# Kernel optimization log

Measured on AMD Instinct MI355X. Metric: run time of the kernel, lower is better.

Reference implementation:

```python
import jax, jax.numpy as jnp
import numpy as np

N = 50000
E = 800000
EL = 100000
IN_CH = 33
HID = 64
OUT = 128
NTYPES = 311
EMB = 16
COMB = IN_CH - 1 + EMB  # 48


def setup_inputs() -> dict:
    key = jax.random.key(0)
    ks = jax.random.split(key, 24)
    # x: col 0 = node type (integer-valued float), rest = float features
    types = jax.random.randint(ks[0], (N, 1), 0, NTYPES).astype(jnp.float32)
    feats = jax.random.normal(ks[1], (N, IN_CH - 1), dtype=jnp.float32)
    x = jnp.concatenate([types, feats], axis=1)
    edge_index = jax.random.randint(ks[2], (2, E), 0, N, dtype=jnp.int32)
    edge_label_index = jax.random.randint(ks[3], (2, EL), 0, N, dtype=jnp.int32)
    s = 0.05
    inp = {
        'x': x, 'edge_index': edge_index, 'edge_label_index': edge_label_index,
        'emb': jax.random.normal(ks[4], (NTYPES, EMB)) * s,
        'W1': jax.random.normal(ks[5], (COMB, 4 * HID)) * s,
        'a_src1': jax.random.normal(ks[6], (4, HID)) * s,
        'a_dst1': jax.random.normal(ks[7], (4, HID)) * s,
        'b1': jnp.zeros((4 * HID,)),
        'W2': jax.random.normal(ks[8], (4 * HID, 2 * 2 * HID)) * s,
        'a_src2': jax.random.normal(ks[9], (2, 2 * HID)) * s,
        'a_dst2': jax.random.normal(ks[10], (2, 2 * HID)) * s,
        'b2': jnp.zeros((2 * 2 * HID,)),
        'W3': jax.random.normal(ks[11], (4 * HID, OUT)) * s,
        'a_src3': jax.random.normal(ks[12], (1, OUT)) * s,
        'a_dst3': jax.random.normal(ks[13], (1, OUT)) * s,
        'b3': jnp.zeros((OUT,)),
        'Wl1': jax.random.normal(ks[14], (2 * OUT, HID)) * s,
        'bl1': jnp.zeros((HID,)),
        'Wl2': jax.random.normal(ks[15], (HID, 1)) * s,
        'bl2': jnp.zeros((1,)),
        'trans_bias': jax.random.normal(ks[16], (NTYPES, NTYPES)) * s,
    }
    return inp


def _gat(h_in, src, dst, W, a_src, a_dst, b, heads, d_out):
    # linear transform, per-head split
    h = (h_in @ W).reshape(N, heads, d_out)                      # [N,H,D]
    al_s = jnp.einsum('nhd,hd->nh', h, a_src)                    # [N,H]
    al_d = jnp.einsum('nhd,hd->nh', h, a_dst)
    logits = jax.nn.leaky_relu(al_s[src] + al_d[dst], 0.2)       # [E,H]
    m = jax.ops.segment_max(logits, dst, num_segments=N)
    m = jnp.where(jnp.isfinite(m), m, 0.0)
    e = jnp.exp(logits - m[dst])
    denom = jax.ops.segment_sum(e, dst, num_segments=N)
    alpha = e / (denom[dst] + 1e-16)                             # [E,H]
    msg = h[src] * alpha[:, :, None]                             # [E,H,D]
    out = jax.ops.segment_sum(msg, dst, num_segments=N)          # [N,H,D]
    return out.reshape(N, heads * d_out) + b


def reference(x, edge_index, edge_label_index, emb, W1, a_src1, a_dst1, b1,
              W2, a_src2, a_dst2, b2, W3, a_src3, a_dst3, b3,
              Wl1, bl1, Wl2, bl2, trans_bias):
    node_types = x[:, 0].astype(jnp.int32)
    x_comb = jnp.concatenate([emb[node_types], x[:, 1:]], axis=1)  # [N,48]
    # add self loops (PyG GATConv default)
    loops = jnp.arange(N, dtype=edge_index.dtype)
    ei = jnp.concatenate([edge_index, jnp.stack([loops, loops])], axis=1)
    src, dst = ei[0], ei[1]
    z = jax.nn.elu(_gat(x_comb, src, dst, W1, a_src1, a_dst1, b1, 4, HID))
    z = jax.nn.elu(_gat(z, src, dst, W2, a_src2, a_dst2, b2, 2, 2 * HID))
    z = _gat(z, src, dst, W3, a_src3, a_dst3, b3, 1, OUT)
    # decode
    ls, ld = edge_label_index[0], edge_label_index[1]
    ef = jnp.concatenate([z[ls], z[ld]], axis=1)                  # [EL,2*OUT]
    h = jax.nn.relu(ef @ Wl1 + bl1)
    base = h @ Wl2 + bl2                                          # [EL,1]
    bias = trans_bias[node_types[ls], node_types[ld]][:, None]
    return base + bias
```

## Files before the change

kernel.cpp:

```cpp
#include <hip/hip_runtime.h>
#include <hip/hip_bf16.h>

#define NN 50000
#define EE 800000
#define ELN 100000
#define ETOT (EE + NN)
#define NT 311

#define NBUCK ((NN + 127) >> 7)
#define BCAP 3072
#define CHUNK 8192

typedef _Float16 f16;
typedef f16 f16x8 __attribute__((ext_vector_type(8)));
typedef f16 f16x4 __attribute__((ext_vector_type(4)));
typedef f16 f16x2 __attribute__((ext_vector_type(2)));
typedef float f32x4 __attribute__((ext_vector_type(4)));

__global__ __launch_bounds__(256) void k_prepatt(const float* __restrict__ x,
                                                 const float* __restrict__ emb,
                                                 const float* __restrict__ a1ps,
                                                 const float* __restrict__ a1pd,
                                                 f16* __restrict__ xc,
                                                 int* __restrict__ ntypes,
                                                 float* __restrict__ als,
                                                 float* __restrict__ ald)
{
    int gid = blockIdx.x * 256 + threadIdx.x;
    int n = gid >> 6, lane = gid & 63;
    if (n >= NN) return;
    int tpe = (int)x[(size_t)n * 33];
    tpe = tpe < 0 ? 0 : (tpe > NT - 1 ? NT - 1 : tpe);
    if (lane == 0) ntypes[n] = tpe;
    float v;
    if (lane < 16)      v = emb[tpe * 16 + lane];
    else if (lane < 48) v = x[(size_t)n * 33 + 1 + (lane - 16)];
    else                v = 0.f;
    f16 hv = (f16)v;
    xc[(size_t)n * 64 + lane] = hv;
    float xv = (float)hv;
    float ps[4], pd[4];
    #pragma unroll
    for (int h = 0; h < 4; ++h) {
        ps[h] = xv * a1ps[h * 64 + lane];
        pd[h] = xv * a1pd[h * 64 + lane];
    }
    #pragma unroll
    for (int off = 32; off > 0; off >>= 1) {
        #pragma unroll
        for (int h = 0; h < 4; ++h) {
            ps[h] += __shfl_xor(ps[h], off, 64);
            pd[h] += __shfl_xor(pd[h], off, 64);
        }
    }
    if (lane == 0) {
        #pragma unroll
        for (int h = 0; h < 4; ++h) {
            als[n * 4 + h] = ps[h];
            ald[n * 4 + h] = pd[h];
        }
    }
}

__global__ __launch_bounds__(256) void k_cvtall(const float* __restrict__ W1,
                                                const float* __restrict__ W2,
                                                const float* __restrict__ W3,
                                                const float* __restrict__ Wl1,
                                                f16* __restrict__ Wt1,
                                                f16* __restrict__ Wt2,
                                                f16* __restrict__ Wt3,
                                                f16* __restrict__ Wtl)
{
    int idx = blockIdx.x * 256 + threadIdx.x;
    if (idx < 16384) {
        int h = idx >> 12, c = (idx >> 6) & 63, k = idx & 63;
        Wt1[idx] = (k < 48) ? (f16)W1[(size_t)k * 256 + h * 64 + c] : (f16)0.f;
    } else if (idx < 81920) {
        int i = idx - 16384;
        int c = i >> 8, k = i & 255;
        Wt2[i] = (f16)W2[(size_t)k * 256 + c];
    } else if (idx < 114688) {
        int i = idx - 81920;
        int c = i >> 8, k = i & 255;
        Wt3[i] = (f16)W3[(size_t)k * 128 + c];
    } else if (idx < 131072) {
        int i = idx - 114688;
        int c = i >> 8, k = i & 255;
        Wtl[i] = (f16)Wl1[(size_t)k * 64 + c];
    }
}

__global__ __launch_bounds__(256) void k_pre1(const float* __restrict__ W1,
                                              const float* __restrict__ as1,
                                              const float* __restrict__ ad1,
                                              float* __restrict__ a1ps,
                                              float* __restrict__ a1pd)
{
    int t = threadIdx.x;
    int h = t >> 6, k = t & 63;
    float ss = 0.f, sd = 0.f;
    if (k < 48) {
        for (int d = 0; d < 64; ++d) {
            float w = W1[(size_t)k * 256 + h * 64 + d];
            ss += w * as1[h * 64 + d];
            sd += w * ad1[h * 64 + d];
        }
    }
    a1ps[t] = ss;
    a1pd[t] = sd;
}

__global__ __launch_bounds__(256) void k_bucket(const int* __restrict__ ei,
                                                int* __restrict__ bcur,
                                                int2* __restrict__ bbuf)
{
    __shared__ int hist[NBUCK];
    __shared__ int gbase[NBUCK];
    const int t = threadIdx.x;
    for (int i = t; i < NBUCK; i += 256) hist[i] = 0;
    __syncthreads();
    const int e0 = blockIdx.x * CHUNK;
    const int eend = min(e0 + CHUNK, ETOT);
    for (int e = e0 + t; e < eend; e += 256) {
        int dst = (e < EE) ? ei[EE + e] : (e - EE);
        atomicAdd(&hist[dst >> 7], 1);
    }
    __syncthreads();
    for (int i = t; i < NBUCK; i += 256) {
        int c = hist[i];
        gbase[i] = c ? atomicAdd(&bcur[i], c) : 0;
        hist[i] = 0;
    }
    __syncthreads();
    for (int e = e0 + t; e < eend; e += 256) {
        int src, dst;
        if (e < EE) { src = ei[e]; dst = ei[EE + e]; }
        else        { src = e - EE; dst = src; }
        int b = dst >> 7;
        int pos = gbase[b] + atomicAdd(&hist[b], 1);
        if (pos < BCAP)
            bbuf[(size_t)b * BCAP + pos] = make_int2(src, dst);
    }
}

__global__ __launch_bounds__(512) void k_bscan(const int* __restrict__ bcur,
                                               int* __restrict__ boff)
{
    __shared__ int s[512];
    int t = threadIdx.x;
    int v = (t < NBUCK) ? min(bcur[t], BCAP) : 0;
    s[t] = v;
    __syncthreads();
    #pragma unroll
    for (int off = 1; off < 512; off <<= 1) {
        int u = (t >= off) ? s[t - off] : 0;
        __syncthreads();
        s[t] += u;
        __syncthreads();
    }
    if (t < NBUCK) boff[t] = s[t] - v;
    if (t == NBUCK - 1) boff[NBUCK] = s[t];
}

__global__ __launch_bounds__(256) void k_csrb(const int* __restrict__ bcur,
                                              const int* __restrict__ boff,
                                              const int2* __restrict__ bbuf,
                                              int* __restrict__ rowptr,
                                              int* __restrict__ csr,
                                              int* __restrict__ dstarr)
{
    __shared__ int nh[128];
    __shared__ int loff[128];
    __shared__ int ncur[128];
    __shared__ int ssrc[BCAP];
    __shared__ int sdst[BCAP];
    const int b = blockIdx.x;
    const int t = threadIdx.x;
    const int n0 = b << 7;
    const int cnt = min(bcur[b], BCAP);
    const int base = boff[b];
    const size_t bb = (size_t)b * BCAP;
    if (t < 128) { nh[t] = 0; ncur[t] = 0; }
    __syncthreads();
    for (int i = t; i < cnt; i += 256)
        atomicAdd(&nh[bbuf[bb + i].y - n0], 1);
    __syncthreads();
    int myc = (t < 128) ? nh[t] : 0;
    #pragma unroll
    for (int off = 1; off < 128; off <<= 1) {
        int u = (t >= off && t < 128) ? nh[t - off] : 0;
        __syncthreads();
        if (t < 128) nh[t] += u;
        __syncthreads();
    }
    if (t < 128) {
        int ex = nh[t] - myc;
        loff[t] = ex;
        int n = n0 + t;
        if (n < NN) rowptr[n] = base + ex;
    }
    __syncthreads();
    for (int i = t; i < cnt; i += 256) {
        int2 p = bbuf[bb + i];
        int ln = p.y - n0;
        int pos = loff[ln] + atomicAdd(&ncur[ln], 1);
        ssrc[pos] = p.x;
        sdst[pos] = p.y;
    }
    __syncthreads();
    for (int i = t; i < cnt; i += 256) {
        csr[base + i]    = ssrc[i];
        dstarr[base + i] = sdst[i];
    }
    if (b == 0 && t == 0) rowptr[NN] = boff[NBUCK];
}

template<int K, int CN, int H>
__global__ __launch_bounds__(256) void k_gemmw(const f16* __restrict__ A,
                                               const f16* __restrict__ Wt,
                                               f16* __restrict__ O,
                                               int nrows,
                                               const float* __restrict__ asrc,
                                               const float* __restrict__ adst,
                                               float* __restrict__ als,
                                               float* __restrict__ ald)
{
    constexpr int LDK = 40;
    __shared__ f16 As[128 * LDK];
    __shared__ f16 Bs[128 * LDK];
    const int t = threadIdx.x;
    const int w = t >> 6;
    const int lane = t & 63;
    const int m = lane & 15;
    const int quad = lane >> 4;
    const int row0 = blockIdx.x * 128;
    const int col0 = blockIdx.y * 128;
    const int r_st = t >> 1;
    const int seg  = (t & 1) * 16;
    f32x4 acc[2][8] = {};
    for (int k0 = 0; k0 < K; k0 += 32) {
        int gr = row0 + r_st;
        f16x8 av0 = {0,0,0,0,0,0,0,0}, av1 = {0,0,0,0,0,0,0,0};
        if (gr < nrows) {
            av0 = *(const f16x8*)&A[(size_t)gr * K + k0 + seg];
            av1 = *(const f16x8*)&A[(size_t)gr * K + k0 + seg + 8];
        }
        *(f16x8*)&As[r_st * LDK + seg]     = av0;
        *(f16x8*)&As[r_st * LDK + seg + 8] = av1;
        f16x8 bv0 = *(const f16x8*)&Wt[(size_t)(col0 + r_st) * K + k0 + seg];
        f16x8 bv1 = *(const f16x8*)&Wt[(size_t)(col0 + r_st) * K + k0 + seg + 8];
        *(f16x8*)&Bs[r_st * LDK + seg]     = bv0;
        *(f16x8*)&Bs[r_st * LDK + seg + 8] = bv1;
        __syncthreads();
        f16x8 af0 = *(const f16x8*)&As[(w * 32 + m) * LDK + quad * 8];
        f16x8 af1 = *(const f16x8*)&As[(w * 32 + 16 + m) * LDK + quad * 8];
        #pragma unroll
        for (int g = 0; g < 8; ++g) {
            f16x8 bf = *(const f16x8*)&Bs[(g * 16 + m) * LDK + quad * 8];
            acc[0][g] = __builtin_amdgcn_mfma_f32_16x16x32_f16(af0, bf, acc[0][g], 0, 0, 0);
            acc[1][g] = __builtin_amdgcn_mfma_f32_16x16x32_f16(af1, bf, acc[1][g], 0, 0, 0);
        }
        __syncthreads();
    }
    #pragma unroll
    for (int rb = 0; rb < 2; ++rb) {
        #pragma unroll
        for (int g = 0; g < 8; ++g) {
            #pragma unroll
            for (int reg = 0; reg < 4; ++reg) {
                int gr = row0 + w * 32 + rb * 16 + quad * 4 + reg;
                int gc = col0 + g * 16 + m;
                if (gr < nrows) O[(size_t)gr * CN + gc] = (f16)acc[rb][g][reg];
            }
        }
    }
    if constexpr (H > 0) {
        constexpr int D = CN / H;
        const int head = col0 / D;
        float ps[2][4] = {}, pd[2][4] = {};
        #pragma unroll
        for (int g = 0; g < 8; ++g) {
            int col = col0 + g * 16 + m;
            float a_s = asrc[col], a_d = adst[col];
            #pragma unroll
            for (int rb = 0; rb < 2; ++rb) {
                #pragma unroll
                for (int reg = 0; reg < 4; ++reg) {
                    ps[rb][reg] += acc[rb][g][reg] * a_s;
                    pd[rb][reg] += acc[rb][g][reg] * a_d;
                }
            }
        }
        #pragma unroll
        for (int off = 1; off < 16; off <<= 1) {
            #pragma unroll
            for (int rb = 0; rb < 2; ++rb) {
                #pragma unroll
                for (int reg = 0; reg < 4; ++reg) {
                    ps[rb][reg] += __shfl_xor(ps[rb][reg], off, 64);
                    pd[rb][reg] += __shfl_xor(pd[rb][reg], off, 64);
                }
            }
        }
        if (m == 0) {
            #pragma unroll
            for (int rb = 0; rb < 2; ++rb) {
                #pragma unroll
                for (int reg = 0; reg < 4; ++reg) {
                    int gr = row0 + w * 32 + rb * 16 + quad * 4 + reg;
                    if (gr < nrows) {
                        atomicAdd(&als[gr * H + head], ps[rb][reg]);
                        atomicAdd(&ald[gr * H + head], pd[rb][reg]);
                    }
                }
            }
        }
    }
}

__global__ __launch_bounds__(256) void k_gemm1h(const f16* __restrict__ A,
                                                const f16* __restrict__ Wt1,
                                                const float* __restrict__ bias,
                                                f16* __restrict__ O,
                                                int nrows)
{
    constexpr int LDA = 40;
    __shared__ f16 As[64 * LDA];
    __shared__ f16 Bs[64 * LDA];
    const int t = threadIdx.x;
    const int w = t >> 6;
    const int lane = t & 63;
    const int m = lane & 15;
    const int quad = lane >> 4;
    const int row0 = blockIdx.x * 64;
    const int head = blockIdx.y;
    const int r_st = t >> 2;
    const int seg  = (t & 3) * 8;
    f32x4 acc[4] = {{0.f,0.f,0.f,0.f},{0.f,0.f,0.f,0.f},{0.f,0.f,0.f,0.f},{0.f,0.f,0.f,0.f}};
    for (int k0 = 0; k0 < 64; k0 += 32) {
        int gr = row0 + r_st;
        f16x8 av = {0,0,0,0,0,0,0,0};
        if (gr < nrows) av = *(const f16x8*)&A[(size_t)gr * 256 + head * 64 + k0 + seg];
        *(f16x8*)&As[r_st * LDA + seg] = av;
        f16x8 bv = *(const f16x8*)&Wt1[(size_t)head * 4096 + (size_t)r_st * 64 + k0 + seg];
        *(f16x8*)&Bs[r_st * LDA + seg] = bv;
        __syncthreads();
        f16x8 af = *(const f16x8*)&As[(w * 16 + m) * LDA + quad * 8];
        #pragma unroll
        for (int g = 0; g < 4; ++g) {
            f16x8 bf = *(const f16x8*)&Bs[(g * 16 + m) * LDA + quad * 8];
            acc[g] = __builtin_amdgcn_mfma_f32_16x16x32_f16(af, bf, acc[g], 0, 0, 0);
        }
        __syncthreads();
    }
    #pragma unroll
    for (int g = 0; g < 4; ++g) {
        #pragma unroll
        for (int reg = 0; reg < 4; ++reg) {
            int gr = row0 + w * 16 + quad * 4 + reg;
            int col = head * 64 + g * 16 + m;
            if (gr < nrows) {
                float v = acc[g][reg] + bias[col];
                v = v > 0.f ? v : (__expf(v) - 1.f);
                O[(size_t)gr * 256 + col] = (f16)v;
            }
        }
    }
}

template<int H>
__global__ __launch_bounds__(256) void k_ew(const int* __restrict__ csr,
                                            const int* __restrict__ dstarr,
                                            const float* __restrict__ als,
                                            const float* __restrict__ ald,
                                            float* __restrict__ earr)
{
    int i = blockIdx.x * 256 + threadIdx.x;
    if (i >= ETOT) return;
    int s = csr[i], d = dstarr[i];
    #pragma unroll
    for (int hh = 0; hh < H; ++hh) {
        float l = als[s * H + hh] + ald[d * H + hh];
        l = l > 0.f ? l : 0.2f * l;
        earr[(size_t)i * H + hh] = __expf(fminf(l, 80.f));
    }
}

__global__ __launch_bounds__(256) void k_aggx(const int* __restrict__ rowptr,
                                              const int* __restrict__ csr,
                                              const float* __restrict__ earr,
                                              const f16* __restrict__ xc,
                                              f16* __restrict__ xagg)
{
    int gid = blockIdx.x * 256 + threadIdx.x;
    int n = gid >> 6, lane = gid & 63;
    if (n >= NN) return;
    int p  = lane >> 4;
    int fl = lane & 15;
    int cb = fl * 4;
    int r0 = rowptr[n], r1 = rowptr[n + 1];
    float a0[4] = {}, a1[4] = {}, a2[4] = {}, a3[4] = {};
    float d0 = 0.f, d1 = 0.f, d2 = 0.f, d3 = 0.f;
    int i = r0;
    for (; i + 8 <= r1; i += 8) {
        int i0 = i + p, i1 = i + 4 + p;
        int s0 = csr[i0], s1 = csr[i1];
        float4 e0 = *(const float4*)&earr[(size_t)i0 * 4];
        float4 e1 = *(const float4*)&earr[(size_t)i1 * 4];
        f16x4 x0 = *(const f16x4*)&xc[(size_t)s0 * 64 + cb];
        f16x4 x1 = *(const f16x4*)&xc[(size_t)s1 * 64 + cb];
        #pragma unroll
        for (int j = 0; j < 4; ++j) {
            float v0 = (float)x0[j], v1 = (float)x1[j];
            a0[j] += e0.x * v0 + e1.x * v1;
            a1[j] += e0.y * v0 + e1.y * v1;
            a2[j] += e0.z * v0 + e1.z * v1;
            a3[j] += e0.w * v0 + e1.w * v1;
        }
        d0 += e0.x + e1.x; d1 += e0.y + e1.y;
        d2 += e0.z + e1.z; d3 += e0.w + e1.w;
    }
    for (; i < r1; i += 4) {
        int ii = i + p;
        bool v = ii < r1;
        int s0 = csr[v ? ii : r0];
        float4 e0 = *(const float4*)&earr[(size_t)(v ? ii : r0) * 4];
        if (!v) { e0.x = 0.f; e0.y = 0.f; e0.z = 0.f; e0.w = 0.f; }
        f16x4 x0 = *(const f16x4*)&xc[(size_t)s0 * 64 + cb];
        #pragma unroll
        for (int j = 0; j < 4; ++j) {
            float v0 = (float)x0[j];
            a0[j] += e0.x * v0; a1[j] += e0.y * v0;
            a2[j] += e0.z * v0; a3[j] += e0.w * v0;
        }
        d0 += e0.x; d1 += e0.y; d2 += e0.z; d3 += e0.w;
    }
    #pragma unroll
    for (int off = 16; off < 64; off <<= 1) {
        #pragma unroll
        for (int j = 0; j < 4; ++j) {
            a0[j] += __shfl_xor(a0[j], off, 64);
            a1[j] += __shfl_xor(a1[j], off, 64);
            a2[j] += __shfl_xor(a2[j], off, 64);
            a3[j] += __shfl_xor(a3[j], off, 64);
        }
        d0 += __shfl_xor(d0, off, 64);
        d1 += __shfl_xor(d1, off, 64);
        d2 += __shfl_xor(d2, off, 64);
        d3 += __shfl_xor(d3, off, 64);
    }
    if (p == 0) {
        float i0 = 1.f / d0, i1 = 1.f / d1, i2 = 1.f / d2, i3 = 1.f / d3;
        size_t base = (size_t)n * 256 + cb;
        f16x4 o0, o1, o2, o3;
        #pragma unroll
        for (int j = 0; j < 4; ++j) {
            o0[j] = (f16)(a0[j] * i0);
            o1[j] = (f16)(a1[j] * i1);
            o2[j] = (f16)(a2[j] * i2);
            o3[j] = (f16)(a3[j] * i3);
        }
        *(f16x4*)&xagg[base]       = o0;
        *(f16x4*)&xagg[base + 64]  = o1;
        *(f16x4*)&xagg[base + 128] = o2;
        *(f16x4*)&xagg[base + 192] = o3;
    }
}

__global__ __launch_bounds__(256) void k_agg2f(const int* __restrict__ rowptr,
                                               const int* __restrict__ csr,
                                               const float* __restrict__ earr,
                                               const f16* __restrict__ h,
                                               const float* __restrict__ bias,
                                               f16* __restrict__ z)
{
    int gid = blockIdx.x * 256 + threadIdx.x;
    int n = gid >> 6, lane = gid & 63;
    if (n >= NN) return;
    int p  = lane >> 5;
    int cb = (lane & 31) * 8;
    int head = cb >> 7;
    int r0 = rowptr[n], r1 = rowptr[n + 1];
    float a[8] = {};
    float den = 0.f;
    int i = r0;
    for (; i + 8 <= r1; i += 8) {
        int i0 = i + p, i1 = i + 2 + p, i2 = i + 4 + p, i3 = i + 6 + p;
        int s0 = csr[i0], s1 = csr[i1], s2 = csr[i2], s3 = csr[i3];
        float e0 = earr[(size_t)i0 * 2 + head];
        float e1 = earr[(size_t)i1 * 2 + head];
        float e2 = earr[(size_t)i2 * 2 + head];
        float e3 = earr[(size_t)i3 * 2 + head];
        f16x8 h0 = *(const f16x8*)&h[(size_t)s0 * 256 + cb];
        f16x8 h1 = *(const f16x8*)&h[(size_t)s1 * 256 + cb];
        f16x8 h2 = *(const f16x8*)&h[(size_t)s2 * 256 + cb];
        f16x8 h3 = *(const f16x8*)&h[(size_t)s3 * 256 + cb];
        #pragma unroll
        for (int j = 0; j < 8; ++j)
            a[j] += e0 * (float)h0[j] + e1 * (float)h1[j]
                  + e2 * (float)h2[j] + e3 * (float)h3[j];
        den += e0 + e1 + e2 + e3;
    }
    for (; i < r1; i += 2) {
        int ii = i + p;
        bool v = ii < r1;
        int s0 = csr[v ? ii : r0];
        float e0 = v ? earr[(size_t)ii * 2 + head] : 0.f;
        f16x8 h0 = *(const f16x8*)&h[(size_t)s0 * 256 + cb];
        #pragma unroll
        for (int j = 0; j < 8; ++j) a[j] += e0 * (float)h0[j];
        den += e0;
    }
    #pragma unroll
    for (int j = 0; j < 8; ++j) a[j] += __shfl_xor(a[j], 32, 64);
    den += __shfl_xor(den, 32, 64);
    if (p == 0) {
        float inv = 1.f / den;
        f16x8 o;
        #pragma unroll
        for (int j = 0; j < 8; ++j) {
            float v = a[j] * inv + bias[cb + j];
            v = v > 0.f ? v : (__expf(v) - 1.f);
            o[j] = (f16)v;
        }
        *(f16x8*)&z[(size_t)n * 256 + cb] = o;
    }
}

__global__ __launch_bounds__(256) void k_agg3(const int* __restrict__ rowptr,
                                              const int* __restrict__ csr,
                                              const float* __restrict__ earr,
                                              const f16* __restrict__ h,
                                              const float* __restrict__ bias,
                                              f16* __restrict__ z)
{
    int gid = blockIdx.x * 256 + threadIdx.x;
    int n = gid >> 6, lane = gid & 63;
    if (n >= NN) return;
    int p  = lane >> 4;
    int cb = (lane & 15) * 8;
    int r0 = rowptr[n], r1 = rowptr[n + 1];
    float a[8] = {};
    float den = 0.f;
    int i = r0;
    for (; i + 8 <= r1; i += 8) {
        int i0 = i + p, i1 = i + 4 + p;
        int s0 = csr[i0], s1 = csr[i1];
        float e0 = earr[i0], e1 = earr[i1];
        f16x8 h0 = *(const f16x8*)&h[(size_t)s0 * 128 + cb];
        f16x8 h1 = *(const f16x8*)&h[(size_t)s1 * 128 + cb];
        #pragma unroll
        for (int j = 0; j < 8; ++j)
            a[j] += e0 * (float)h0[j] + e1 * (float)h1[j];
        den += e0 + e1;
    }
    for (; i < r1; i += 4) {
        int ii = i + p;
        bool v = ii < r1;
        int s0 = csr[v ? ii : r0];
        float e0 = v ? earr[ii] : 0.f;
        f16x8 h0 = *(const f16x8*)&h[(size_t)s0 * 128 + cb];
        #pragma unroll
        for (int j = 0; j < 8; ++j) a[j] += e0 * (float)h0[j];
        den += e0;
    }
    #pragma unroll
    for (int j = 0; j < 8; ++j) {
        a[j] += __shfl_xor(a[j], 16, 64);
        a[j] += __shfl_xor(a[j], 32, 64);
    }
    den += __shfl_xor(den, 16, 64);
    den += __shfl_xor(den, 32, 64);
    if (lane < 16) {
        float inv = 1.f / den;
        f16x8 o;
        #pragma unroll
        for (int j = 0; j < 8; ++j)
            o[j] = (f16)(a[j] * inv + bias[cb + j]);
        *(f16x8*)&z[(size_t)n * 128 + cb] = o;
    }
}

#define DLDA 264
__global__ __launch_bounds__(256) void k_decm(const f16* __restrict__ z3,
                                              const int* __restrict__ eli,
                                              const int* __restrict__ ntypes,
                                              const f16* __restrict__ Wtl,
                                              const float* __restrict__ bl1,
                                              const float* __restrict__ Wl2,
                                              const float* __restrict__ bl2,
                                              const float* __restrict__ tb,
                                              float* __restrict__ out)
{
    __shared__ f16 As[64 * DLDA];
    __shared__ int sls[64], sld[64];
    const int t = threadIdx.x;
    const int e0 = blockIdx.x * 64;
    if (t < 64) {
        int e = e0 + t;
        sls[t] = (e < ELN) ? eli[e] : 0;
        sld[t] = (e < ELN) ? eli[ELN + e] : 0;
    }
    __syncthreads();
    {
        int r = t & 63;
        int seg = t >> 6;
        int base = seg * 64;
        int node = (base < 128) ? sls[r] : sld[r];
        int zoff = base & 127;
        #pragma unroll
        for (int j = 0; j < 8; ++j) {
            f16x8 v = *(const f16x8*)&z3[(size_t)node * 128 + zoff + j * 8];
            *(f16x8*)&As[r * DLDA + base + j * 8] = v;
        }
    }
    __syncthreads();
    const int w = t >> 6;
    const int lane = t & 63;
    const int m = lane & 15;
    const int quad = lane >> 4;
    f32x4 acc[4] = {{0.f,0.f,0.f,0.f},{0.f,0.f,0.f,0.f},{0.f,0.f,0.f,0.f},{0.f,0.f,0.f,0.f}};
    for (int k0 = 0; k0 < 256; k0 += 32) {
        f16x8 af = *(const f16x8*)&As[(w * 16 + m) * DLDA + k0 + quad * 8];
        #pragma unroll
        for (int g = 0; g < 4; ++g) {
            f16x8 bf = *(const f16x8*)&Wtl[(size_t)(g * 16 + m) * 256 + k0 + quad * 8];
            acc[g] = __builtin_amdgcn_mfma_f32_16x16x32_f16(af, bf, acc[g], 0, 0, 0);
        }
    }
    float s[4] = {0.f, 0.f, 0.f, 0.f};
    #pragma unroll
    for (int g = 0; g < 4; ++g) {
        int col = g * 16 + m;
        float b = bl1[col], wv = Wl2[col];
        #pragma unroll
        for (int reg = 0; reg < 4; ++reg) {
            float hv = fmaxf(acc[g][reg] + b, 0.f);
            s[reg] += hv * wv;
        }
    }
    #pragma unroll
    for (int off = 1; off < 16; off <<= 1) {
        #pragma unroll
        for (int reg = 0; reg < 4; ++reg) s[reg] += __shfl_xor(s[reg], off, 64);
    }
    if (m == 0) {
        float b2v = bl2[0];
        #pragma unroll
        for (int reg = 0; reg < 4; ++reg) {
            int r = w * 16 + quad * 4 + reg;
            int e = e0 + r;
            if (e < ELN) {
                out[e] = s[reg] + b2v +
                         tb[(size_t)ntypes[sls[r]] * NT + ntypes[sld[r]]];
            }
        }
    }
}

extern "C" void kernel_launch(void* const* d_in, const int* in_sizes, int n_in,
                              void* d_out, int out_size, void* d_ws, size_t ws_size,
                              hipStream_t stream)
{
    const float* x   = (const float*)d_in[0];
    const int*   ei  = (const int*)d_in[1];
    const int*   eli = (const int*)d_in[2];
    const float* emb = (const float*)d_in[3];
    const float* W1  = (const float*)d_in[4];
    const float* as1 = (const float*)d_in[5];
    const float* ad1 = (const float*)d_in[6];
    const float* b1  = (const float*)d_in[7];
    const float* W2  = (const float*)d_in[8];
    const float* as2 = (const float*)d_in[9];
    const float* ad2 = (const float*)d_in[10];
    const float* b2  = (const float*)d_in[11];
    const float* W3  = (const float*)d_in[12];
    const float* as3 = (const float*)d_in[13];
    const float* ad3 = (const float*)d_in[14];
    const float* b3  = (const float*)d_in[15];
    const float* Wl1 = (const float*)d_in[16];
    const float* bl1 = (const float*)d_in[17];
    const float* Wl2 = (const float*)d_in[18];
    const float* bl2 = (const float*)d_in[19];
    const float* tb  = (const float*)d_in[20];
    float* out = (float*)d_out;

    char* ws = (char*)d_ws;
    size_t off = 0;
    auto alloc = [&](size_t bytes) { size_t o = off; off = (off + bytes + 255) & ~(size_t)255; return o; };
    int*   ntypes = (int*)  (ws + alloc((size_t)NN * 4));
    f16*   xc16   = (f16*)  (ws + alloc((size_t)NN * 64 * 2));
    int*   rowptr = (int*)  (ws + alloc((size_t)(NN + 1) * 4));
    int*   csr    = (int*)  (ws + alloc((size_t)ETOT * 4));
    int*   dstarr = (int*)  (ws + alloc((size_t)ETOT * 4));
    int*   bcur   = (int*)  (ws + alloc((size_t)(NBUCK + 1) * 4));
    int*   boff   = (int*)  (ws + alloc((size_t)(NBUCK + 1) * 4));
    float* scores = (float*)(ws + alloc((size_t)NN * 14 * 4));
    float* als1 = scores;
    float* ald1 = scores + (size_t)NN * 4;
    float* als2 = scores + (size_t)NN * 8;
    float* ald2 = scores + (size_t)NN * 10;
    float* als3 = scores + (size_t)NN * 12;
    float* ald3 = scores + (size_t)NN * 13;
    float* earr   = (float*)(ws + alloc((size_t)ETOT * 4 * 4));
    f16*   h16    = (f16*)  (ws + alloc((size_t)NN * 256 * 2));
    f16*   z16    = (f16*)  (ws + alloc((size_t)NN * 256 * 2));
    f16*   Wt1    = (f16*)  (ws + alloc((size_t)4 * 64 * 64 * 2));
    f16*   Wt2    = (f16*)  (ws + alloc((size_t)256 * 256 * 2));
    f16*   Wt3    = (f16*)  (ws + alloc((size_t)128 * 256 * 2));
    f16*   Wtl    = (f16*)  (ws + alloc((size_t)64 * 256 * 2));
    float* a1ps   = (float*)(ws + alloc(256 * 4));
    float* a1pd   = (float*)(ws + alloc(256 * 4));

    int2* bbuf = (int2*)earr;

    hipMemsetAsync(bcur, 0, (size_t)(NBUCK + 1) * 4, stream);
    hipMemsetAsync(als2, 0, (size_t)NN * 6 * 4, stream);

    const int gE   = (ETOT + 255) / 256;
    const int RB   = (NN + 63) / 64;
    const int RB2  = (NN + 127) / 128;
    const int gW1  = (NN + 3) / 4;

    k_pre1<<<1, 256, 0, stream>>>(W1, as1, ad1, a1ps, a1pd);
    k_prepatt<<<gW1, 256, 0, stream>>>(x, emb, a1ps, a1pd, xc16, ntypes, als1, ald1);
    k_cvtall<<<(131072 + 255) / 256, 256, 0, stream>>>(W1, W2, W3, Wl1, Wt1, Wt2, Wt3, Wtl);

    k_bucket<<<(ETOT + CHUNK - 1) / CHUNK, 256, 0, stream>>>(ei, bcur, bbuf);
    k_bscan <<<1, 512, 0, stream>>>(bcur, boff);
    k_csrb  <<<NBUCK, 256, 0, stream>>>(bcur, boff, bbuf, rowptr, csr, dstarr);

    k_ew<4><<<gE, 256, 0, stream>>>(csr, dstarr, als1, ald1, earr);
    k_aggx<<<gW1, 256, 0, stream>>>(rowptr, csr, earr, xc16, h16 );
    k_gemm1h<<<dim3(RB, 4), 256, 0, stream>>>(h16 , Wt1, b1, z16, NN);

    k_gemmw<256, 256, 2><<<dim3(RB2, 2), 256, 0, stream>>>(z16, Wt2, h16, NN, as2, ad2, als2, ald2);
    k_ew<2><<<gE, 256, 0, stream>>>(csr, dstarr, als2, ald2, earr);
    k_agg2f<<<gW1, 256, 0, stream>>>(rowptr, csr, earr, h16, b2, z16);

    k_gemmw<256, 128, 1><<<dim3(RB2, 1), 256, 0, stream>>>(z16, Wt3, h16, NN, as3, ad3, als3, ald3);
    k_ew<1><<<gE, 256, 0, stream>>>(csr, dstarr, als3, ald3, earr);
    k_agg3<<<gW1, 256, 0, stream>>>(rowptr, csr, earr, h16, b3, z16);

    k_decm<<<(ELN + 63) / 64, 256, 0, stream>>>(z16, eli, ntypes, Wtl, bl1, Wl2, bl2, tb, out);
}
```

Baseline: 411.1 us.

## Fuse edge attention weight computation into aggregation kernels, drop edge arrays

Removes the three separate per-edge exp kernels and the materialized edge-weight array. Each aggregation kernel now computes leaky-relu and exp on the fly from per-node source and destination scores. The CSR build no longer writes a destination array, and the bucket buffer gets its own allocation instead of aliasing the edge array. This cuts three launches and roughly the write and read traffic of the edge weights, but adds redundant exp work, since several lanes compute the same weight, plus extra gathers of source scores.

Result: faster. 397.2 us (-3.4%).

```diff
diff --git a/kernel.cpp b/kernel.cpp
--- a/kernel.cpp
+++ b/kernel.cpp
@@ -16,6 +16,12 @@
 typedef f16 f16x4 __attribute__((ext_vector_type(4)));
 typedef f16 f16x2 __attribute__((ext_vector_type(2)));
 typedef float f32x4 __attribute__((ext_vector_type(4)));
+
+__device__ __forceinline__ float edge_alpha(float l)
+{
+    l = l > 0.f ? l : 0.2f * l;
+    return __expf(fminf(l, 80.f));
+}
 
 __global__ __launch_bounds__(256) void k_prepatt(const float* __restrict__ x,
                                                  const float* __restrict__ emb,
@@ -166,14 +172,12 @@
                                               const int* __restrict__ boff,
                                               const int2* __restrict__ bbuf,
                                               int* __restrict__ rowptr,
-                                              int* __restrict__ csr,
-                                              int* __restrict__ dstarr)
+                                              int* __restrict__ csr)
 {
     __shared__ int nh[128];
     __shared__ int loff[128];
     __shared__ int ncur[128];
     __shared__ int ssrc[BCAP];
-    __shared__ int sdst[BCAP];
     const int b = blockIdx.x;
     const int t = threadIdx.x;
     const int n0 = b << 7;
@@ -205,13 +209,10 @@
         int ln = p.y - n0;
         int pos = loff[ln] + atomicAdd(&ncur[ln], 1);
         ssrc[pos] = p.x;
-        sdst[pos] = p.y;
-    }
-    __syncthreads();
-    for (int i = t; i < cnt; i += 256) {
-        csr[base + i]    = ssrc[i];
-        dstarr[base + i] = sdst[i];
-    }
+    }
+    __syncthreads();
+    for (int i = t; i < cnt; i += 256)
+        csr[base + i] = ssrc[i];
     if (b == 0 && t == 0) rowptr[NN] = boff[NBUCK];
 }
 
@@ -368,27 +369,10 @@
     }
 }
 
-template<int H>
-__global__ __launch_bounds__(256) void k_ew(const int* __restrict__ csr,
-                                            const int* __restrict__ dstarr,
-                                            const float* __restrict__ als,
-                                            const float* __restrict__ ald,
-                                            float* __restrict__ earr)
-{
-    int i = blockIdx.x * 256 + threadIdx.x;
-    if (i >= ETOT) return;
-    int s = csr[i], d = dstarr[i];
-    #pragma unroll
-    for (int hh = 0; hh < H; ++hh) {
-        float l = als[s * H + hh] + ald[d * H + hh];
-        l = l > 0.f ? l : 0.2f * l;
-        earr[(size_t)i * H + hh] = __expf(fminf(l, 80.f));
-    }
-}
-
 __global__ __launch_bounds__(256) void k_aggx(const int* __restrict__ rowptr,
                                               const int* __restrict__ csr,
-                                              const float* __restrict__ earr,
+                                              const float* __restrict__ als,
+                                              const float* __restrict__ ald,
                                               const f16* __restrict__ xc,
                                               f16* __restrict__ xagg)
 {
@@ -399,16 +383,22 @@
     int fl = lane & 15;
     int cb = fl * 4;
     int r0 = rowptr[n], r1 = rowptr[n + 1];
+    float4 dl = *(const float4*)&ald[(size_t)n * 4];
     float a0[4] = {}, a1[4] = {}, a2[4] = {}, a3[4] = {};
     float d0 = 0.f, d1 = 0.f, d2 = 0.f, d3 = 0.f;
     int i = r0;
     for (; i + 8 <= r1; i += 8) {
         int i0 = i + p, i1 = i + 4 + p;
         int s0 = csr[i0], s1 = csr[i1];
-        float4 e0 = *(const float4*)&earr[(size_t)i0 * 4];
-        float4 e1 = *(const float4*)&earr[(size_t)i1 * 4];
         f16x4 x0 = *(const f16x4*)&xc[(size_t)s0 * 64 + cb];
         f16x4 x1 = *(const f16x4*)&xc[(size_t)s1 * 64 + cb];
+        float4 A0 = *(const float4*)&als[(size_t)s0 * 4];
+        float4 A1 = *(const float4*)&als[(size_t)s1 * 4];
+        float4 e0, e1;
+        e0.x = edge_alpha(A0.x + dl.x); e1.x = edge_alpha(A1.x + dl.x);
+        e0.y = edge_alpha(A0.y + dl.y); e1.y = edge_alpha(A1.y + dl.y);
+        e0.z = edge_alpha(A0.z + dl.z); e1.z = edge_alpha(A1.z + dl.z);
+        e0.w = edge_alpha(A0.w + dl.w); e1.w = edge_alpha(A1.w + dl.w);
         #pragma unroll
         for (int j = 0; j < 4; ++j) {
             float v0 = (float)x0[j], v1 = (float)x1[j];
@@ -424,9 +414,13 @@
         int ii = i + p;
         bool v = ii < r1;
         int s0 = csr[v ? ii : r0];
-        float4 e0 = *(const float4*)&earr[(size_t)(v ? ii : r0) * 4];
-        if (!v) { e0.x = 0.f; e0.y = 0.f; e0.z = 0.f; e0.w = 0.f; }
         f16x4 x0 = *(const f16x4*)&xc[(size_t)s0 * 64 + cb];
+        float4 A0 = *(const float4*)&als[(size_t)s0 * 4];
+        float4 e0;
+        e0.x = v ? edge_alpha(A0.x + dl.x) : 0.f;
+        e0.y = v ? edge_alpha(A0.y + dl.y) : 0.f;
+        e0.z = v ? edge_alpha(A0.z + dl.z) : 0.f;
+        e0.w = v ? edge_alpha(A0.w + dl.w) : 0.f;
         #pragma unroll
         for (int j = 0; j < 4; ++j) {
             float v0 = (float)x0[j];
@@ -469,7 +463,8 @@
 
 __global__ __launch_bounds__(256) void k_agg2f(const int* __restrict__ rowptr,
                                                const int* __restrict__ csr,
-                                               const float* __restrict__ earr,
+                                               const float* __restrict__ als,
+                                               const float* __restrict__ ald,
                                                const f16* __restrict__ h,
                                                const float* __restrict__ bias,
                                                f16* __restrict__ z)
@@ -481,20 +476,25 @@
     int cb = (lane & 31) * 8;
     int head = cb >> 7;
     int r0 = rowptr[n], r1 = rowptr[n + 1];
+    float dd = ald[(size_t)n * 2 + head];
     float a[8] = {};
     float den = 0.f;
     int i = r0;
     for (; i + 8 <= r1; i += 8) {
         int i0 = i + p, i1 = i + 2 + p, i2 = i + 4 + p, i3 = i + 6 + p;
         int s0 = csr[i0], s1 = csr[i1], s2 = csr[i2], s3 = csr[i3];
-        float e0 = earr[(size_t)i0 * 2 + head];
-        float e1 = earr[(size_t)i1 * 2 + head];
-        float e2 = earr[(size_t)i2 * 2 + head];
-        float e3 = earr[(size_t)i3 * 2 + head];
         f16x8 h0 = *(const f16x8*)&h[(size_t)s0 * 256 + cb];
         f16x8 h1 = *(const f16x8*)&h[(size_t)s1 * 256 + cb];
         f16x8 h2 = *(const f16x8*)&h[(size_t)s2 * 256 + cb];
         f16x8 h3 = *(const f16x8*)&h[(size_t)s3 * 256 + cb];
+        float w0 = als[(size_t)s0 * 2 + head];
+        float w1 = als[(size_t)s1 * 2 + head];
+        float w2 = als[(size_t)s2 * 2 + head];
+        float w3 = als[(size_t)s3 * 2 + head];
+        float e0 = edge_alpha(w0 + dd);
+        float e1 = edge_alpha(w1 + dd);
+        float e2 = edge_alpha(w2 + dd);
+        float e3 = edge_alpha(w3 + dd);
         #pragma unroll
         for (int j = 0; j < 8; ++j)
             a[j] += e0 * (float)h0[j] + e1 * (float)h1[j]
@@ -505,8 +505,8 @@
         int ii = i + p;
         bool v = ii < r1;
         int s0 = csr[v ? ii : r0];
-        float e0 = v ? earr[(size_t)ii * 2 + head] : 0.f;
         f16x8 h0 = *(const f16x8*)&h[(size_t)s0 * 256 + cb];
+        float e0 = v ? edge_alpha(als[(size_t)s0 * 2 + head] + dd) : 0.f;
         #pragma unroll
         for (int j = 0; j < 8; ++j) a[j] += e0 * (float)h0[j];
         den += e0;
@@ -529,7 +529,8 @@
 
 __global__ __launch_bounds__(256) void k_agg3(const int* __restrict__ rowptr,
                                               const int* __restrict__ csr,
-                                              const float* __restrict__ earr,
+                                              const float* __restrict__ als,
+                                              const float* __restrict__ ald,
                                               const f16* __restrict__ h,
                                               const float* __restrict__ bias,
                                               f16* __restrict__ z)
@@ -540,15 +541,17 @@
     int p  = lane >> 4;
     int cb = (lane & 15) * 8;
     int r0 = rowptr[n], r1 = rowptr[n + 1];
+    float dd = ald[n];
     float a[8] = {};
     float den = 0.f;
     int i = r0;
     for (; i + 8 <= r1; i += 8) {
         int i0 = i + p, i1 = i + 4 + p;
         int s0 = csr[i0], s1 = csr[i1];
-        float e0 = earr[i0], e1 = earr[i1];
         f16x8 h0 = *(const f16x8*)&h[(size_t)s0 * 128 + cb];
         f16x8 h1 = *(const f16x8*)&h[(size_t)s1 * 128 + cb];
+        float e0 = edge_alpha(als[s0] + dd);
+        float e1 = edge_alpha(als[s1] + dd);
         #pragma unroll
         for (int j = 0; j < 8; ++j)
             a[j] += e0 * (float)h0[j] + e1 * (float)h1[j];
@@ -558,8 +561,8 @@
         int ii = i + p;
         bool v = ii < r1;
         int s0 = csr[v ? ii : r0];
-        float e0 = v ? earr[ii] : 0.f;
         f16x8 h0 = *(const f16x8*)&h[(size_t)s0 * 128 + cb];
+        float e0 = v ? edge_alpha(als[s0] + dd) : 0.f;
         #pragma unroll
         for (int j = 0; j < 8; ++j) a[j] += e0 * (float)h0[j];
         den += e0;
@@ -692,7 +695,6 @@
     f16*   xc16   = (f16*)  (ws + alloc((size_t)NN * 64 * 2));
     int*   rowptr = (int*)  (ws + alloc((size_t)(NN + 1) * 4));
     int*   csr    = (int*)  (ws + alloc((size_t)ETOT * 4));
-    int*   dstarr = (int*)  (ws + alloc((size_t)ETOT * 4));
     int*   bcur   = (int*)  (ws + alloc((size_t)(NBUCK + 1) * 4));
     int*   boff   = (int*)  (ws + alloc((size_t)(NBUCK + 1) * 4));
     float* scores = (float*)(ws + alloc((size_t)NN * 14 * 4));
@@ -702,7 +704,7 @@
     float* ald2 = scores + (size_t)NN * 10;
     float* als3 = scores + (size_t)NN * 12;
     float* ald3 = scores + (size_t)NN * 13;
-    float* earr   = (float*)(ws + alloc((size_t)ETOT * 4 * 4));
+    int2*  bbuf   = (int2*) (ws + alloc((size_t)NBUCK * BCAP * 8));
     f16*   h16    = (f16*)  (ws + alloc((size_t)NN * 256 * 2));
     f16*   z16    = (f16*)  (ws + alloc((size_t)NN * 256 * 2));
     f16*   Wt1    = (f16*)  (ws + alloc((size_t)4 * 64 * 64 * 2));
@@ -712,12 +714,9 @@
     float* a1ps   = (float*)(ws + alloc(256 * 4));
     float* a1pd   = (float*)(ws + alloc(256 * 4));
 
-    int2* bbuf = (int2*)earr;
-
     hipMemsetAsync(bcur, 0, (size_t)(NBUCK + 1) * 4, stream);
     hipMemsetAsync(als2, 0, (size_t)NN * 6 * 4, stream);
 
-    const int gE   = (ETOT + 255) / 256;
     const int RB   = (NN + 63) / 64;
     const int RB2  = (NN + 127) / 128;
     const int gW1  = (NN + 3) / 4;
@@ -728,19 +727,16 @@
 
     k_bucket<<<(ETOT + CHUNK - 1) / CHUNK, 256, 0, stream>>>(ei, bcur, bbuf);
     k_bscan <<<1, 512, 0, stream>>>(bcur, boff);
-    k_csrb  <<<NBUCK, 256, 0, stream>>>(bcur, boff, bbuf, rowptr, csr, dstarr);
-
-    k_ew<4><<<gE, 256, 0, stream>>>(csr, dstarr, als1, ald1, earr);
-    k_aggx<<<gW1, 256, 0, stream>>>(rowptr, csr, earr, xc16, h16 );
+    k_csrb  <<<NBUCK, 256, 0, stream>>>(bcur, boff, bbuf, rowptr, csr);
+
+    k_aggx<<<gW1, 256, 0, stream>>>(rowptr, csr, als1, ald1, xc16, h16 );
     k_gemm1h<<<dim3(RB, 4), 256, 0, stream>>>(h16 , Wt1, b1, z16, NN);
 
     k_gemmw<256, 256, 2><<<dim3(RB2, 2), 256, 0, stream>>>(z16, Wt2, h16, NN, as2, ad2, als2, ald2);
-    k_ew<2><<<gE, 256, 0, stream>>>(csr, dstarr, als2, ald2, earr);
-    k_agg2f<<<gW1, 256, 0, stream>>>(rowptr, csr, earr, h16, b2, z16);
+    k_agg2f<<<gW1, 256, 0, stream>>>(rowptr, csr, als2, ald2, h16, b2, z16);
 
     k_gemmw<256, 128, 1><<<dim3(RB2, 1), 256, 0, stream>>>(z16, Wt3, h16, NN, as3, ad3, als3, ald3);
-    k_ew<1><<<gE, 256, 0, stream>>>(csr, dstarr, als3, ald3, earr);
-    k_agg3<<<gW1, 256, 0, stream>>>(rowptr, csr, earr, h16, b3, z16);
+    k_agg3<<<gW1, 256, 0, stream>>>(rowptr, csr, als3, ald3, h16, b3, z16);
 
     k_decm<<<(ELN + 63) / 64, 256, 0, stream>>>(z16, eli, ntypes, Wtl, bl1, Wl2, bl2, tb, out);
 }
```
